# Optimization experiments

Measured on AMD Instinct MI355X. Metric: run time of the kernel, lower is better.

## Reference

```python
import jax, jax.numpy as jnp
import numpy as np

BS, D_NUM, SLEN, DIM = 64, 2, 50, 64   # batch, domains, history len, embedding_dim
NUM_EMB = 512                          # codebook size (hardcoded in source)
NEG_INF = -1e30                        # stand-in for -np.inf (NaN-safe under softmax grad)


def setup_inputs() -> dict:
    key = jax.random.key(0)
    ks = jax.random.split(key, 16)
    w = lambda k, shape: jax.random.normal(k, shape, jnp.float32) * 0.05
    inp = {
        "x": jax.random.normal(ks[0], (BS, D_NUM, SLEN, DIM), jnp.float32),
        "code_book": jax.random.normal(ks[1], (NUM_EMB, DIM), jnp.float32) * 0.1,
        "Wq_is": w(ks[2], (DIM, DIM)), "bq_is": jnp.zeros((DIM,), jnp.float32),
        "Wk_is": w(ks[3], (DIM, DIM)), "bk_is": jnp.zeros((DIM,), jnp.float32),
        "Wv_is": w(ks[4], (DIM, DIM)), "bv_is": jnp.zeros((DIM,), jnp.float32),
        "Wq_cs": w(ks[5], (DIM, DIM)), "bq_cs": jnp.zeros((DIM,), jnp.float32),
        "Wk_cs": w(ks[6], (DIM, DIM)), "bk_cs": jnp.zeros((DIM,), jnp.float32),
        "Wv_cs": w(ks[7], (DIM, DIM)), "bv_cs": jnp.zeros((DIM,), jnp.float32),
    }
    return inp


def reference(x, code_book,
              Wq_is, bq_is, Wk_is, bk_is, Wv_is, bv_is,
              Wq_cs, bq_cs, Wk_cs, bk_cs, Wv_cs, bv_cs):
    bs, dn, sl, dim = x.shape
    flat = x.reshape(-1, dim)  # [N, dim], N = bs*dn*sl

    # ---- get_quantized: cdist + argmin + codebook lookup ----
    # ||f||^2 + ||c||^2 - 2 f c^T, argmin over codebook, gather (== one_hot @ code_book)
    dists = (jnp.sum(flat * flat, axis=1, keepdims=True)
             + jnp.sum(code_book * code_book, axis=1)
             - 2.0 * flat @ code_book.T)                      # [N, NUM_EMB]
    idx = jnp.argmin(dists, axis=1)                           # [N]
    quantized = code_book[idx].reshape(x.shape)               # [bs, dn, sl, dim]

    # ---- intra-sample (IS) attention: softmax(K Q^T) V per (sample, domain) ----
    q = (flat @ Wq_is + bq_is).reshape(bs, dn, sl, dim)
    k = (flat @ Wk_is + bk_is).reshape(bs, dn, sl, dim)
    v = (flat @ Wv_is + bv_is).reshape(bs, dn, sl, dim)
    is_kq = jnp.einsum('bdse,bdte->bdst', k, q)               # K @ Q^T, [bs, dn, sl, sl]
    Z = jnp.einsum('bdst,bdte->bdse', jax.nn.softmax(is_kq, axis=-1), v)

    # ---- cross-sample (CS) attention: dense NxN, own-sample block masked out ----
    qc = flat @ Wq_cs + bq_cs                                  # [N, dim]
    kc = flat @ Wk_cs + bk_cs
    vc = flat @ Wv_cs + bv_cs
    sid = jnp.repeat(jnp.arange(bs), dn * sl)                  # sample id per row
    same = sid[:, None] == sid[None, :]                        # block-diagonal mask
    scores = kc @ qc.T                                         # [N, N]
    scores = jnp.where(same, NEG_INF, scores)                  # mask own-sample block
    X = (jax.nn.softmax(scores, axis=-1) @ vc).reshape(x.shape)

    return quantized, Z, X
```

## Files before the change

### kernel.cpp

```cpp
#include <hip/hip_runtime.h>
#include <hip/hip_bf16.h>
#include <math.h>

#define DIM 64
#define NROW 6400
#define SLEN 50
#define NG 128
#define NEMB 512
#define SAMPLE 100
#define NCHUNK 100
#define NQB 400
#define SMAX 7
#define LOG2E 1.4426950408889634f
#define SM_SHIFT2 11.541560327111707f
#define LSTR 72

typedef unsigned short ushort_t;
typedef __attribute__((ext_vector_type(8))) short short8;
typedef __attribute__((ext_vector_type(4))) float floatx4;

__device__ __forceinline__ ushort_t f2bu(float f) {
    __hip_bfloat16 h = __float2bfloat16(f);
    ushort_t u;
    __builtin_memcpy(&u, &h, 2);
    return u;
}

__device__ __forceinline__ float fast_exp2(float x) {
#if __has_builtin(__builtin_amdgcn_exp2f)
    return __builtin_amdgcn_exp2f(x);
#else
    return exp2f(x);
#endif
}

__global__ __launch_bounds__(256)
void projprep_kernel(const float* __restrict__ x,
                     const float* __restrict__ W0, const float* __restrict__ W1,
                     const float* __restrict__ W2, const float* __restrict__ W3,
                     const float* __restrict__ W4, const float* __restrict__ W5,
                     const float* __restrict__ b0, const float* __restrict__ b1,
                     const float* __restrict__ b2, const float* __restrict__ b3,
                     const float* __restrict__ b4, const float* __restrict__ b5,
                     const float* __restrict__ cb, float* __restrict__ cbT,
                     double* __restrict__ c2,
                     ushort_t* __restrict__ qib, ushort_t* __restrict__ kib,
                     ushort_t* __restrict__ vib,
                     ushort_t* __restrict__ qcb, ushort_t* __restrict__ kcb,
                     ushort_t* __restrict__ vtb)
{
    const int tid = threadIdx.x;

    if (blockIdx.x >= 200) {
        const int c = (blockIdx.x - 200) * 256 + tid;
        const float* cr = cb + (size_t)c * DIM;
        double s = 0.0;
#pragma unroll 8
        for (int e = 0; e < DIM; ++e) {
            const float v = cr[e];
            cbT[(size_t)e * NEMB + c] = v;
            s = fma((double)v, (double)v, s);
        }
        c2[c] = s;
        return;
    }

    __shared__ __align__(16) ushort_t Xb[64 * LSTR];
    __shared__ __align__(16) ushort_t WL[64 * LSTR];

    const int wave = tid >> 6, lane = tid & 63;
    const int col = lane & 15;
    const int quad = lane >> 4;

    const int r0 = (blockIdx.x >> 1) * 64;
    const int pbase = (blockIdx.x & 1) * 3;

    const float* Ws[6] = {W0, W1, W2, W3, W4, W5};
    const float* Bs[6] = {b0, b1, b2, b3, b4, b5};

    const int kr = tid >> 2, seg = tid & 3;

    {
        const float* src = x + (size_t)(r0 + kr) * DIM + seg * 16;
        ushort_t* dst = &Xb[kr * LSTR + seg * 16];
#pragma unroll
        for (int i = 0; i < 16; ++i) dst[i] = f2bu(src[i]);
    }

    short8 aX0, aX1;

#pragma unroll
    for (int pp = 0; pp < 3; ++pp) {
        const int p = pbase + pp;
        const float scale = (p == 1 || p == 4) ? LOG2E : 1.0f;

        if (pp) __syncthreads();
        {
            const float* wrow = Ws[p] + (size_t)kr * DIM + seg * 16;
            float wv[16];
#pragma unroll
            for (int i = 0; i < 16; ++i) wv[i] = wrow[i];
#pragma unroll
            for (int i = 0; i < 16; ++i)
                WL[(seg * 16 + i) * LSTR + kr] = f2bu(wv[i] * scale);
        }
        __syncthreads();

        if (pp == 0) {
            aX0 = *(const short8*)&Xb[(wave * 16 + col) * LSTR + quad * 8];
            aX1 = *(const short8*)&Xb[(wave * 16 + col) * LSTR + quad * 8 + 32];
        }

#pragma unroll
        for (int nt = 0; nt < 4; ++nt) {
            const int n = nt * 16 + col;
            float bv = Bs[p][n];
            if (p == 1 || p == 4) bv *= LOG2E;
            floatx4 c = (floatx4){bv, bv, bv, bv};
            const ushort_t* wr = &WL[n * LSTR + quad * 8];
            const short8 w0 = *(const short8*)wr;
            const short8 w1 = *(const short8*)(wr + 32);
            c = __builtin_amdgcn_mfma_f32_16x16x32_bf16(aX0, w0, c, 0, 0, 0);
            c = __builtin_amdgcn_mfma_f32_16x16x32_bf16(aX1, w1, c, 0, 0, 0);
#pragma unroll
            for (int r = 0; r < 4; ++r) {
                const int row = r0 + wave * 16 + quad * 4 + r;
                const ushort_t ub = f2bu(c[r]);
                if (p == 0)      qib[(size_t)row * DIM + n] = ub;
                else if (p == 1) kib[(size_t)row * DIM + n] = ub;
                else if (p == 2) vib[(size_t)row * DIM + n] = ub;
                else if (p == 3) qcb[(size_t)row * DIM + n] = ub;
                else if (p == 4) kcb[(size_t)row * DIM + n] = ub;
                else             vtb[(size_t)n * NROW + row] = ub;
            }
        }
    }
}

__global__ __launch_bounds__(256, 5)
void attn_quant_kernel(const ushort_t* __restrict__ qib, const ushort_t* __restrict__ kib,
                       const ushort_t* __restrict__ vib, float* __restrict__ outZ,
                       const ushort_t* __restrict__ qcb, const ushort_t* __restrict__ kcb,
                       const ushort_t* __restrict__ vtb,
                       float* __restrict__ pl, float* __restrict__ pacc,
                       float* __restrict__ outX,
                       const float* __restrict__ x, const float* __restrict__ cb,
                       const float* __restrict__ cbT, const double* __restrict__ c2,
                       float* __restrict__ outq,
                       int S, int direct)
{
    __shared__ __align__(16) ushort_t smem[3 * 64 * LSTR];

    const int tid = threadIdx.x;
    const int wave = tid >> 6;
    const int lane = tid & 63;

    if ((int)blockIdx.x < NQB) {
        const int r0 = blockIdx.x * 16;

        double* xs    = (double*)smem;
        double* candd = xs + 16 * 64;
        int*    candi = (int*)(candd + 64);
        int*    sidx  = candi + 64;

        for (int idx = tid; idx < 16 * DIM; idx += 256) {
            const int r = idx >> 6, e = idx & 63;
            xs[r * 64 + e] = (double)x[(size_t)(r0 + r) * DIM + e];
        }
        __syncthreads();

        const int c0 = wave * 64 + lane;
        double dot0[16], dot1[16];
#pragma unroll
        for (int r = 0; r < 16; ++r) { dot0[r] = 0.0; dot1[r] = 0.0; }

        for (int e = 0; e < DIM; ++e) {
            const double ce0 = (double)cbT[(size_t)e * NEMB + c0];
            const double ce1 = (double)cbT[(size_t)e * NEMB + c0 + 256];
#pragma unroll
            for (int r = 0; r < 16; ++r) {
                const double xe = xs[r * 64 + e];
                dot0[r] = fma(xe, ce0, dot0[r]);
                dot1[r] = fma(xe, ce1, dot1[r]);
            }
        }

        const double cc0 = c2[c0];
        const double cc1 = c2[c0 + 256];
#pragma unroll
        for (int r = 0; r < 16; ++r) {
            double bd = cc0 - 2.0 * dot0[r];
            int bi = c0;
            const double d1 = cc1 - 2.0 * dot1[r];
            if (d1 < bd) { bd = d1; bi = c0 + 256; }
            for (int off = 32; off; off >>= 1) {
                const double od = __shfl_down(bd, off, 64);
                const int oi = __shfl_down(bi, off, 64);
                if (od < bd || (od == bd && oi < bi)) { bd = od; bi = oi; }
            }
            if (lane == 0) { candd[wave * 16 + r] = bd; candi[wave * 16 + r] = bi; }
        }
        __syncthreads();
        if (tid < 16) {
            double bd = candd[tid];
            int bi = candi[tid];
#pragma unroll
            for (int w = 1; w < 4; ++w) {
                const double od = candd[w * 16 + tid];
                const int oi = candi[w * 16 + tid];
                if (od < bd || (od == bd && oi < bi)) { bd = od; bi = oi; }
            }
            sidx[tid] = bi;
        }
        __syncthreads();
        for (int idx = tid; idx < 16 * DIM; idx += 256) {
            const int r = idx >> 6, e = idx & 63;
            outq[(size_t)(r0 + r) * DIM + e] = cb[(size_t)sidx[r] * DIM + e];
        }
        return;
    }

    const int ab = blockIdx.x - NQB;
    const int col = lane & 15;
    const int quad = lane >> 4;

    short8 ones;
#pragma unroll
    for (int i = 0; i < 8; ++i) ones[i] = (short)0x3F80;

    if (ab < 100 * S) {
        const int bi = ab / S;
        const int split = ab % S;
        const int i0 = bi * 64 + wave * 16;

        ushort_t* Qs = smem;
        ushort_t* Vs = smem + 64 * LSTR;
        ushort_t* Pb = smem + 2 * 64 * LSTR + wave * 16 * LSTR;

        const int srow = tid >> 2;
        const int sseg = tid & 3;

        short8 aK0, aK1;
        {
            const ushort_t* kr = kcb + (size_t)(i0 + col) * DIM + quad * 8;
            aK0 = *(const short8*)kr;
            aK1 = *(const short8*)(kr + 32);
        }

        int lo[4];
        float l[4];
        floatx4 O[4];
#pragma unroll
        for (int r = 0; r < 4; ++r) {
            lo[r] = ((i0 + quad * 4 + r) / SAMPLE) * SAMPLE;
            l[r] = 0.f;
        }
#pragma unroll
        for (int et = 0; et < 4; ++et) O[et] = (floatx4){0.f, 0.f, 0.f, 0.f};

        {
            const int j0 = split * 64;
            const uint4* qsrc = (const uint4*)(qcb + (size_t)(j0 + srow) * DIM + sseg * 16);
            const uint4* vsrc = (const uint4*)(vtb + (size_t)srow * NROW + j0 + sseg * 16);
            const uint4 q0 = qsrc[0], q1 = qsrc[1];
            const uint4 v0 = vsrc[0], v1 = vsrc[1];
            uint4* qdst = (uint4*)&Qs[srow * LSTR + sseg * 16];
            uint4* vdst = (uint4*)&Vs[srow * LSTR + sseg * 16];
            qdst[0] = q0; qdst[1] = q1;
            vdst[0] = v0; vdst[1] = v1;
        }
        __syncthreads();

        for (int ch = split; ch < NCHUNK; ch += S) {
            const int nxt = ch + S;
            uint4 q0, q1, v0, v1;
            if (nxt < NCHUNK) {
                const int j0n = nxt * 64;
                const uint4* qsrc = (const uint4*)(qcb + (size_t)(j0n + srow) * DIM + sseg * 16);
                const uint4* vsrc = (const uint4*)(vtb + (size_t)srow * NROW + j0n + sseg * 16);
                q0 = qsrc[0]; q1 = qsrc[1];
                v0 = vsrc[0]; v1 = vsrc[1];
            }

            const int j0 = ch * 64;

            floatx4 Sv[4];
#pragma unroll
            for (int jt = 0; jt < 4; ++jt) {
                const short8 b0 = *(const short8*)&Qs[(jt * 16 + col) * LSTR + quad * 8];
                const short8 b1 = *(const short8*)&Qs[(jt * 16 + col) * LSTR + quad * 8 + 32];
                floatx4 c = (floatx4){0.f, 0.f, 0.f, 0.f};
                c = __builtin_amdgcn_mfma_f32_16x16x32_bf16(aK0, b0, c, 0, 0, 0);
                c = __builtin_amdgcn_mfma_f32_16x16x32_bf16(aK1, b1, c, 0, 0, 0);
                Sv[jt] = c;
            }

#pragma unroll
            for (int jt = 0; jt < 4; ++jt) {
                const int jj = j0 + jt * 16 + col;
#pragma unroll
                for (int r = 0; r < 4; ++r) {
                    float p = fast_exp2(Sv[jt][r] - SM_SHIFT2);
                    if ((unsigned)(jj - lo[r]) < SAMPLE) p = 0.f;
                    Pb[(quad * 4 + r) * LSTR + jt * 16 + col] = f2bu(p);
                }
            }

            const short8 aP0 = *(const short8*)&Pb[col * LSTR + quad * 8];
            const short8 aP1 = *(const short8*)&Pb[col * LSTR + quad * 8 + 32];

            floatx4 rsv = (floatx4){0.f, 0.f, 0.f, 0.f};
            rsv = __builtin_amdgcn_mfma_f32_16x16x32_bf16(aP0, ones, rsv, 0, 0, 0);
            rsv = __builtin_amdgcn_mfma_f32_16x16x32_bf16(aP1, ones, rsv, 0, 0, 0);
#pragma unroll
            for (int r = 0; r < 4; ++r) l[r] += rsv[r];

#pragma unroll
            for (int et = 0; et < 4; ++et) {
                const short8 b0 = *(const short8*)&Vs[(et * 16 + col) * LSTR + quad * 8];
                const short8 b1 = *(const short8*)&Vs[(et * 16 + col) * LSTR + quad * 8 + 32];
                O[et] = __builtin_amdgcn_mfma_f32_16x16x32_bf16(aP0, b0, O[et], 0, 0, 0);
                O[et] = __builtin_amdgcn_mfma_f32_16x16x32_bf16(aP1, b1, O[et], 0, 0, 0);
            }

            if (nxt < NCHUNK) {
                __syncthreads();
                uint4* qdst = (uint4*)&Qs[srow * LSTR + sseg * 16];
                uint4* vdst = (uint4*)&Vs[srow * LSTR + sseg * 16];
                qdst[0] = q0; qdst[1] = q1;
                vdst[0] = v0; vdst[1] = v1;
                __syncthreads();
            }
        }

        if (direct) {
#pragma unroll
            for (int et = 0; et < 4; ++et)
#pragma unroll
                for (int r = 0; r < 4; ++r)
                    outX[(size_t)(i0 + quad * 4 + r) * DIM + et * 16 + col] = O[et][r] / l[r];
        } else {
#pragma unroll
            for (int et = 0; et < 4; ++et)
#pragma unroll
                for (int r = 0; r < 4; ++r)
                    pacc[((size_t)split * NROW + i0 + quad * 4 + r) * DIM + et * 16 + col] = O[et][r];
            if (col == 0) {
#pragma unroll
                for (int r = 0; r < 4; ++r)
                    pl[(size_t)split * NROW + i0 + quad * 4 + r] = l[r];
            }
        }
    } else {
        const int g = ab - 100 * S;
        const size_t base = (size_t)g * SLEN * DIM;

        ushort_t* Vt = smem;
        ushort_t* Pb = smem + 64 * LSTR + wave * 16 * LSTR;

        {
            const int r = tid >> 2, seg = tid & 3;
            if (r < SLEN) {
                const uint4* vsrc = (const uint4*)(vib + base + (size_t)r * DIM + seg * 16);
                uint4 vv[2] = {vsrc[0], vsrc[1]};
                ushort_t vtmp[16];
                __builtin_memcpy(vtmp, vv, 32);
#pragma unroll
                for (int i = 0; i < 16; ++i)
                    Vt[(seg * 16 + i) * LSTR + r] = vtmp[i];
            } else {
#pragma unroll
                for (int i = 0; i < 16; ++i)
                    Vt[(seg * 16 + i) * LSTR + r] = 0;
            }
        }
        __syncthreads();

        short8 aK0, aK1;
        {
            const ushort_t* kr = kib + base + (size_t)(wave * 16 + col) * DIM + quad * 8;
            aK0 = *(const short8*)kr;
            aK1 = *(const short8*)(kr + 32);
        }

        floatx4 Sv[4];
#pragma unroll
        for (int jt = 0; jt < 4; ++jt) {
            const ushort_t* qr = qib + base + (size_t)(jt * 16 + col) * DIM + quad * 8;
            const short8 q0 = *(const short8*)qr;
            const short8 q1 = *(const short8*)(qr + 32);
            floatx4 c = (floatx4){0.f, 0.f, 0.f, 0.f};
            c = __builtin_amdgcn_mfma_f32_16x16x32_bf16(aK0, q0, c, 0, 0, 0);
            c = __builtin_amdgcn_mfma_f32_16x16x32_bf16(aK1, q1, c, 0, 0, 0);
            Sv[jt] = c;
        }

#pragma unroll
        for (int jt = 0; jt < 4; ++jt) {
            const int t = jt * 16 + col;
#pragma unroll
            for (int r = 0; r < 4; ++r) {
                float p = fast_exp2(Sv[jt][r] - SM_SHIFT2);
                if (t >= SLEN) p = 0.f;
                Pb[(quad * 4 + r) * LSTR + jt * 16 + col] = f2bu(p);
            }
        }

        const short8 aP0 = *(const short8*)&Pb[col * LSTR + quad * 8];
        const short8 aP1 = *(const short8*)&Pb[col * LSTR + quad * 8 + 32];

        floatx4 rsv = (floatx4){0.f, 0.f, 0.f, 0.f};
        rsv = __builtin_amdgcn_mfma_f32_16x16x32_bf16(aP0, ones, rsv, 0, 0, 0);
        rsv = __builtin_amdgcn_mfma_f32_16x16x32_bf16(aP1, ones, rsv, 0, 0, 0);

#pragma unroll
        for (int et = 0; et < 4; ++et) {
            const short8 v0 = *(const short8*)&Vt[(et * 16 + col) * LSTR + quad * 8];
            const short8 v1 = *(const short8*)&Vt[(et * 16 + col) * LSTR + quad * 8 + 32];
            floatx4 o = (floatx4){0.f, 0.f, 0.f, 0.f};
            o = __builtin_amdgcn_mfma_f32_16x16x32_bf16(aP0, v0, o, 0, 0, 0);
            o = __builtin_amdgcn_mfma_f32_16x16x32_bf16(aP1, v1, o, 0, 0, 0);
#pragma unroll
            for (int r = 0; r < 4; ++r) {
                const int s = wave * 16 + quad * 4 + r;
                if (s < SLEN)
                    outZ[base + (size_t)s * DIM + et * 16 + col] = o[r] / rsv[r];
            }
        }
    }
}

__global__ __launch_bounds__(256)
void cs_combine_kernel(const float* __restrict__ pl, const float* __restrict__ pacc,
                       float* __restrict__ outX, int S)
{
    const int row = blockIdx.x * 4 + (threadIdx.x >> 6);
    const int lane = threadIdx.x & 63;
    float l = 0.f, a = 0.f;
    for (int p = 0; p < S; ++p) {
        l += pl[(size_t)p * NROW + row];
        a += pacc[((size_t)p * NROW + row) * DIM + lane];
    }
    outX[(size_t)row * DIM + lane] = a / l;
}

extern "C" void kernel_launch(void* const* d_in, const int* in_sizes, int n_in,
                              void* d_out, int out_size, void* d_ws, size_t ws_size,
                              hipStream_t stream)
{
    (void)in_sizes; (void)n_in; (void)out_size;

    const float* x     = (const float*)d_in[0];
    const float* cb    = (const float*)d_in[1];
    const float* Wq_is = (const float*)d_in[2];  const float* bq_is = (const float*)d_in[3];
    const float* Wk_is = (const float*)d_in[4];  const float* bk_is = (const float*)d_in[5];
    const float* Wv_is = (const float*)d_in[6];  const float* bv_is = (const float*)d_in[7];
    const float* Wq_cs = (const float*)d_in[8];  const float* bq_cs = (const float*)d_in[9];
    const float* Wk_cs = (const float*)d_in[10]; const float* bk_cs = (const float*)d_in[11];
    const float* Wv_cs = (const float*)d_in[12]; const float* bv_cs = (const float*)d_in[13];

    float* outQ = (float*)d_out;
    float* outZ = outQ + (size_t)NROW * DIM;
    float* outX = outZ + (size_t)NROW * DIM;

    const size_t RB    = (size_t)NROW * DIM * sizeof(ushort_t);
    const size_t CBT_B = (size_t)NEMB * DIM * sizeof(float);
    const size_t C2_B  = (size_t)NEMB * sizeof(double);
    const size_t BASE  = 6 * RB + CBT_B + C2_B;
    const size_t PER_SPLIT = (size_t)NROW * DIM * sizeof(float)
                           + (size_t)NROW * sizeof(float);
    int S = 1;
    if (ws_size > BASE) {
        const size_t avail = (ws_size - BASE) / PER_SPLIT;
        S = (avail >= SMAX) ? SMAX : (avail < 1 ? 1 : (int)avail);
    }
    const int direct = (S == 1);

    ushort_t* qib = (ushort_t*)d_ws;
    ushort_t* kib = qib + (size_t)NROW * DIM;
    ushort_t* vib = kib + (size_t)NROW * DIM;
    ushort_t* qcb = vib + (size_t)NROW * DIM;
    ushort_t* kcb = qcb + (size_t)NROW * DIM;
    ushort_t* vtb = kcb + (size_t)NROW * DIM;
    float*    cbT = (float*)((char*)d_ws + 6 * RB);
    double*   c2  = (double*)((char*)d_ws + 6 * RB + CBT_B);
    float*    pacc = (float*)((char*)d_ws + BASE);
    float*    pl   = pacc + (size_t)S * NROW * DIM;

    projprep_kernel<<<202, 256, 0, stream>>>(x,
        Wq_is, Wk_is, Wv_is, Wq_cs, Wk_cs, Wv_cs,
        bq_is, bk_is, bv_is, bq_cs, bk_cs, bv_cs,
        cb, cbT, c2,
        qib, kib, vib, qcb, kcb, vtb);

    attn_quant_kernel<<<NQB + 100 * S + NG, 256, 0, stream>>>(qib, kib, vib, outZ,
                                                              qcb, kcb, vtb,
                                                              pl, pacc, outX,
                                                              x, cb, cbT, c2, outQ,
                                                              S, direct);
    if (!direct)
        cs_combine_kernel<<<NROW / 4, 256, 0, stream>>>(pl, pacc, outX, S);
}
```

Baseline: 60.33 us.

## Load V fragments directly from global into registers, drop V shared tile

The cross-sample attention loop no longer stages the transposed V chunk through shared memory. Each wave loads its V MFMA operand fragments straight from global memory (L2-resident) in two halves around the softmax step. This shrinks LDS per block by a third and raises the occupancy hint from 5 to 6 blocks, with the maximum split count SMAX raised from 7 to 10. In exchange, all four waves now load the same V data redundantly from global, and more registers are live across the loop.

Measured after the change: 110.0 us. +82.3%, slower.

```diff
diff --git a/kernel.cpp b/kernel.cpp
--- a/kernel.cpp
+++ b/kernel.cpp
@@ -10,7 +10,7 @@
 #define SAMPLE 100
 #define NCHUNK 100
 #define NQB 400
-#define SMAX 7
+#define SMAX 10
 #define LOG2E 1.4426950408889634f
 #define SM_SHIFT2 11.541560327111707f
 #define LSTR 72
@@ -137,7 +137,7 @@
     }
 }
 
-__global__ __launch_bounds__(256, 5)
+__global__ __launch_bounds__(256, 6)
 void attn_quant_kernel(const ushort_t* __restrict__ qib, const ushort_t* __restrict__ kib,
                        const ushort_t* __restrict__ vib, float* __restrict__ outZ,
                        const ushort_t* __restrict__ qcb, const ushort_t* __restrict__ kcb,
@@ -149,7 +149,7 @@
                        float* __restrict__ outq,
                        int S, int direct)
 {
-    __shared__ __align__(16) ushort_t smem[3 * 64 * LSTR];
+    __shared__ __align__(16) ushort_t smem[2 * 64 * LSTR];
 
     const int tid = threadIdx.x;
     const int wave = tid >> 6;
@@ -234,8 +234,7 @@
         const int i0 = bi * 64 + wave * 16;
 
         ushort_t* Qs = smem;
-        ushort_t* Vs = smem + 64 * LSTR;
-        ushort_t* Pb = smem + 2 * 64 * LSTR + wave * 16 * LSTR;
+        ushort_t* Pb = smem + 64 * LSTR + wave * 16 * LSTR;
 
         const int srow = tid >> 2;
         const int sseg = tid & 3;
@@ -261,28 +260,29 @@
         {
             const int j0 = split * 64;
             const uint4* qsrc = (const uint4*)(qcb + (size_t)(j0 + srow) * DIM + sseg * 16);
-            const uint4* vsrc = (const uint4*)(vtb + (size_t)srow * NROW + j0 + sseg * 16);
             const uint4 q0 = qsrc[0], q1 = qsrc[1];
-            const uint4 v0 = vsrc[0], v1 = vsrc[1];
             uint4* qdst = (uint4*)&Qs[srow * LSTR + sseg * 16];
-            uint4* vdst = (uint4*)&Vs[srow * LSTR + sseg * 16];
             qdst[0] = q0; qdst[1] = q1;
-            vdst[0] = v0; vdst[1] = v1;
         }
         __syncthreads();
 
         for (int ch = split; ch < NCHUNK; ch += S) {
             const int nxt = ch + S;
-            uint4 q0, q1, v0, v1;
+            const int j0 = ch * 64;
+
+            short8 vf0[2][2];
+#pragma unroll
+            for (int et = 0; et < 2; ++et) {
+                const ushort_t* vr = vtb + (size_t)(et * 16 + col) * NROW + j0 + quad * 8;
+                vf0[et][0] = *(const short8*)vr;
+                vf0[et][1] = *(const short8*)(vr + 32);
+            }
+
+            uint4 q0, q1;
             if (nxt < NCHUNK) {
-                const int j0n = nxt * 64;
-                const uint4* qsrc = (const uint4*)(qcb + (size_t)(j0n + srow) * DIM + sseg * 16);
-                const uint4* vsrc = (const uint4*)(vtb + (size_t)srow * NROW + j0n + sseg * 16);
+                const uint4* qsrc = (const uint4*)(qcb + (size_t)(nxt * 64 + srow) * DIM + sseg * 16);
                 q0 = qsrc[0]; q1 = qsrc[1];
-                v0 = vsrc[0]; v1 = vsrc[1];
-            }
-
-            const int j0 = ch * 64;
+            }
 
             floatx4 Sv[4];
 #pragma unroll
@@ -306,6 +306,14 @@
                 }
             }
 
+            short8 vf1[2][2];
+#pragma unroll
+            for (int et = 0; et < 2; ++et) {
+                const ushort_t* vr = vtb + (size_t)((et + 2) * 16 + col) * NROW + j0 + quad * 8;
+                vf1[et][0] = *(const short8*)vr;
+                vf1[et][1] = *(const short8*)(vr + 32);
+            }
+
             const short8 aP0 = *(const short8*)&Pb[col * LSTR + quad * 8];
             const short8 aP1 = *(const short8*)&Pb[col * LSTR + quad * 8 + 32];
 
@@ -315,20 +323,19 @@
 #pragma unroll
             for (int r = 0; r < 4; ++r) l[r] += rsv[r];
 
-#pragma unroll
-            for (int et = 0; et < 4; ++et) {
-                const short8 b0 = *(const short8*)&Vs[(et * 16 + col) * LSTR + quad * 8];
-                const short8 b1 = *(const short8*)&Vs[(et * 16 + col) * LSTR + quad * 8 + 32];
-                O[et] = __builtin_amdgcn_mfma_f32_16x16x32_bf16(aP0, b0, O[et], 0, 0, 0);
-                O[et] = __builtin_amdgcn_mfma_f32_16x16x32_bf16(aP1, b1, O[et], 0, 0, 0);
-            }
+            O[0] = __builtin_amdgcn_mfma_f32_16x16x32_bf16(aP0, vf0[0][0], O[0], 0, 0, 0);
+            O[0] = __builtin_amdgcn_mfma_f32_16x16x32_bf16(aP1, vf0[0][1], O[0], 0, 0, 0);
+            O[1] = __builtin_amdgcn_mfma_f32_16x16x32_bf16(aP0, vf0[1][0], O[1], 0, 0, 0);
+            O[1] = __builtin_amdgcn_mfma_f32_16x16x32_bf16(aP1, vf0[1][1], O[1], 0, 0, 0);
+            O[2] = __builtin_amdgcn_mfma_f32_16x16x32_bf16(aP0, vf1[0][0], O[2], 0, 0, 0);
+            O[2] = __builtin_amdgcn_mfma_f32_16x16x32_bf16(aP1, vf1[0][1], O[2], 0, 0, 0);
+            O[3] = __builtin_amdgcn_mfma_f32_16x16x32_bf16(aP0, vf1[1][0], O[3], 0, 0, 0);
+            O[3] = __builtin_amdgcn_mfma_f32_16x16x32_bf16(aP1, vf1[1][1], O[3], 0, 0, 0);
 
             if (nxt < NCHUNK) {
                 __syncthreads();
                 uint4* qdst = (uint4*)&Qs[srow * LSTR + sseg * 16];
-                uint4* vdst = (uint4*)&Vs[srow * LSTR + sseg * 16];
                 qdst[0] = q0; qdst[1] = q1;
-                vdst[0] = v0; vdst[1] = v1;
                 __syncthreads();
             }
         }
```
